# Kernel optimization log

Measured on AMD Instinct MI355X. Metric: run time of the kernel, lower is better.

## Reference

```python
import jax, jax.numpy as jnp
import numpy as np

N_NODES = 100000
N_EDGES = 1200000


def gcn_conv(h, W, b, src, dst, n_nodes):
    """PyG GCNConv: h' = D^-1/2 (A+I) D^-1/2 (h W) + b, with self-loops."""
    h = h @ W  # [N, out]
    # degree on A + I (count of incoming edges at dst, plus self-loop)
    deg = jnp.zeros((n_nodes,), h.dtype).at[dst].add(1.0) + 1.0
    dis = jax.lax.rsqrt(deg)  # deg^-1/2, deg >= 1 so safe
    norm = dis[src] * dis[dst]  # [E]
    out = jnp.zeros_like(h).at[dst].add(norm[:, None] * h[src])
    out = out + (1.0 / deg)[:, None] * h  # self-loop term: dis_i^2 * h_i
    return out + b


def global_features(x, T_norm):
    # matches compute_global_features; torch uses .item() so these are constants
    n_comp = jnp.sum(x[:, 2])
    n_AND = jnp.sum(x[:, 3])
    n_OR = jnp.sum(x[:, 4])
    mask = (x[:, 2] == 1.0).astype(x.dtype)
    msum = jnp.sum(mask)
    safe = jnp.maximum(msum, 1.0)
    avg_lambda = jnp.where(msum > 0, jnp.sum(x[:, 0] * mask) / safe, 0.0)
    avg_mu = jnp.where(msum > 0, jnp.sum(x[:, 1] * mask) / safe, 0.0)
    depth = n_AND + n_OR
    g = jnp.stack([n_comp, n_AND, n_OR, depth, avg_lambda, avg_mu, T_norm])[None, :]
    return jax.lax.stop_gradient(g)


def setup_inputs() -> dict:
    key = jax.random.key(0)
    ks = jax.random.split(key, 8)
    x = jax.random.normal(ks[0], (N_NODES, 5), jnp.float32)
    edge_index = jax.random.randint(ks[1], (2, N_EDGES), 0, N_NODES, jnp.int64)
    sc = lambda f: 1.0 / np.sqrt(f)
    return {
        "x": x,
        "edge_index": edge_index,
        "W1": jax.random.normal(ks[2], (5, 64), jnp.float32) * sc(5),
        "b1": jnp.zeros((64,), jnp.float32),
        "W2": jax.random.normal(ks[3], (64, 64), jnp.float32) * sc(64),
        "b2": jnp.zeros((64,), jnp.float32),
        "Wp1": jax.random.normal(ks[4], (71, 32), jnp.float32) * sc(71),
        "bp1": jnp.zeros((32,), jnp.float32),
        "Wp2": jax.random.normal(ks[5], (32, 2), jnp.float32) * sc(32),
        "bp2": jnp.zeros((2,), jnp.float32),
        "T": 100,
        "T_max": 500,
    }


def reference(x, edge_index, W1, b1, W2, b2, Wp1, bp1, Wp2, bp2, T, T_max):
    src, dst = edge_index[0], edge_index[1]
    n = x.shape[0]
    h = jax.nn.relu(gcn_conv(x, W1, b1, src, dst, n))
    h = jax.nn.relu(gcn_conv(h, W2, b2, src, dst, n))
    embedding = jnp.mean(h, axis=0, keepdims=True)  # global_mean_pool, single graph
    T_norm = jnp.asarray(T, x.dtype) / jnp.asarray(T_max, x.dtype)
    g = global_features(x, T_norm)
    e = jnp.concatenate([embedding, g], axis=1)  # [1, 71]
    raw = jax.nn.relu(e @ Wp1 + bp1) @ Wp2 + bp2  # [1, 2]
    return 2.0 + jax.nn.sigmoid(raw) * 4.0
```

## Files before the change

kernel.cpp:

```cpp
#include <hip/hip_runtime.h>
#include <hip/hip_bf16.h>

#define N_NODES_C 100000
#define N_EDGES_C 1200000
#define NB2 98
#define SUBCAP2 1792

typedef unsigned int uint32;
typedef __attribute__((ext_vector_type(8))) short bf16x8;
typedef __attribute__((ext_vector_type(4))) float f32x4;
typedef __attribute__((ext_vector_type(2))) float f32x2;

__device__ __forceinline__ float bf_lo(uint32 u) { return __uint_as_float(u << 16); }
__device__ __forceinline__ float bf_hi(uint32 u) { return __uint_as_float(u & 0xffff0000u); }
__device__ __forceinline__ uint32 bf16r(float f) {
    uint32 u = __float_as_uint(f);
    return (u + 0x7fffu + ((u >> 16) & 1u)) >> 16;
}
__device__ __forceinline__ uint32 pack2(float lo, float hi) {
    return bf16r(lo) | (bf16r(hi) << 16);
}

__global__ void bucket_kernel(const int4* __restrict__ src4, const int4* __restrict__ dst4,
                              int* __restrict__ bcnt, uint32* __restrict__ bedges, int nE4) {
    __shared__ int cntL[NB2];
    __shared__ int baseL[NB2];
    int tid = threadIdx.x;
    int i = blockIdx.x * 256 + tid;
    int sub = blockIdx.x & 7;
    for (int t = tid; t < NB2; t += 256) cntL[t] = 0;
    __syncthreads();
    int4 s4 = make_int4(0, 0, 0, 0), d4 = make_int4(0, 0, 0, 0);
    int b0 = 0, b1 = 0, b2 = 0, b3 = 0;
    bool act = i < nE4;
    if (act) {
        s4 = src4[i];
        d4 = dst4[i];
        b0 = d4.x >> 10; b1 = d4.y >> 10; b2 = d4.z >> 10; b3 = d4.w >> 10;
        atomicAdd(&cntL[b0], 1); atomicAdd(&cntL[b1], 1);
        atomicAdd(&cntL[b2], 1); atomicAdd(&cntL[b3], 1);
    }
    __syncthreads();
    for (int t = tid; t < NB2; t += 256) {
        int n = cntL[t];
        baseL[t] = n ? atomicAdd(&bcnt[sub * NB2 + t], n) : 0;
    }
    __syncthreads();
    for (int t = tid; t < NB2; t += 256) cntL[t] = 0;
    __syncthreads();
    if (act) {
        int o, slot;
        o = atomicAdd(&cntL[b0], 1); slot = baseL[b0] + o;
        if (slot < SUBCAP2)
            bedges[((size_t)b0 * 8 + sub) * SUBCAP2 + slot] =
                (uint32)s4.x | ((uint32)(d4.x & 1023) << 17);
        o = atomicAdd(&cntL[b1], 1); slot = baseL[b1] + o;
        if (slot < SUBCAP2)
            bedges[((size_t)b1 * 8 + sub) * SUBCAP2 + slot] =
                (uint32)s4.y | ((uint32)(d4.y & 1023) << 17);
        o = atomicAdd(&cntL[b2], 1); slot = baseL[b2] + o;
        if (slot < SUBCAP2)
            bedges[((size_t)b2 * 8 + sub) * SUBCAP2 + slot] =
                (uint32)s4.z | ((uint32)(d4.z & 1023) << 17);
        o = atomicAdd(&cntL[b3], 1); slot = baseL[b3] + o;
        if (slot < SUBCAP2)
            bedges[((size_t)b3 * 8 + sub) * SUBCAP2 + slot] =
                (uint32)s4.w | ((uint32)(d4.w & 1023) << 17);
    }
}

__global__ void bscan2_kernel(const int* __restrict__ bcnt, int* __restrict__ boff) {
    __shared__ int sm[128];
    int tid = threadIdx.x;
    int t = 0;
    if (tid < NB2) {
#pragma unroll
        for (int s = 0; s < 8; ++s) t += bcnt[s * NB2 + tid];
    }
    sm[tid] = t;
    __syncthreads();
    for (int off = 1; off < 128; off <<= 1) {
        int v = (tid >= off) ? sm[tid - off] : 0;
        __syncthreads();
        sm[tid] += v;
        __syncthreads();
    }
    if (tid < NB2) boff[tid] = sm[tid] - t;
}

__global__ void __launch_bounds__(1024)
bin3_kernel(const uint32* __restrict__ bedges, const int* __restrict__ bcnt,
            const int* __restrict__ boff, int* __restrict__ rowptr,
            float* __restrict__ dis, int* __restrict__ csr_src, int nN) {
    __shared__ int lc[1024];
    __shared__ int sm[1024];
    __shared__ int pr[1024];
    __shared__ int ln[8];
    int b = blockIdx.x;
    int tid = threadIdx.x;
    lc[tid] = 0;
    if (tid < 8) ln[tid] = min(bcnt[tid * NB2 + b], SUBCAP2);
    __syncthreads();
    const uint32* be = bedges + (size_t)b * 8 * SUBCAP2;
#pragma unroll
    for (int s = 0; s < 8; ++s) {
        int n = ln[s];
        const uint32* bs = be + s * SUBCAP2;
        for (int i = tid; i < n; i += 1024) atomicAdd(&lc[bs[i] >> 17], 1);
    }
    __syncthreads();
    int myc = lc[tid];
    sm[tid] = myc;
    __syncthreads();
    for (int off = 1; off < 1024; off <<= 1) {
        int v = (tid >= off) ? sm[tid - off] : 0;
        __syncthreads();
        sm[tid] += v;
        __syncthreads();
    }
    int excl = sm[tid] - myc;
    int base = boff[b];
    pr[tid] = base + excl;
    int node = (b << 10) + tid;
    if (node <= nN) rowptr[node] = base + excl;
    if (node < nN) dis[node] = rsqrtf((float)(myc + 1));
    lc[tid] = 0;
    __syncthreads();
#pragma unroll
    for (int s = 0; s < 8; ++s) {
        int n = ln[s];
        const uint32* bs = be + s * SUBCAP2;
        for (int i = tid; i < n; i += 1024) {
            uint32 ed = bs[i];
            int dlow = ed >> 17;
            int slot = pr[dlow] + atomicAdd(&lc[dlow], 1);
            csr_src[slot] = ed & 0x1FFFF;
        }
    }
}

__global__ void lin1_kernel(const float* __restrict__ x, const float* __restrict__ W1,
                            const float* __restrict__ dis, uint32* __restrict__ hlin, int nN) {
    __shared__ float Ws[320];
    int tid = threadIdx.x;
    if (tid < 256) Ws[tid] = W1[tid];
    if (tid < 64)  Ws[256 + tid] = W1[256 + tid];
    __syncthreads();
    int q = tid & 15;
    int sub = tid >> 4;
    for (int node = blockIdx.x * 16 + sub; node < nN; node += gridDim.x * 16) {
        const float* xr = x + node * 5;
        float x0 = xr[0], x1 = xr[1], x2 = xr[2], x3 = xr[3], x4 = xr[4];
        float dn = dis[node];
        int j = 4 * q;
        float a0 = x0 * Ws[j+0] + x1 * Ws[64+j+0] + x2 * Ws[128+j+0] + x3 * Ws[192+j+0] + x4 * Ws[256+j+0];
        float a1 = x0 * Ws[j+1] + x1 * Ws[64+j+1] + x2 * Ws[128+j+1] + x3 * Ws[192+j+1] + x4 * Ws[256+j+1];
        float a2 = x0 * Ws[j+2] + x1 * Ws[64+j+2] + x2 * Ws[128+j+2] + x3 * Ws[192+j+2] + x4 * Ws[256+j+2];
        float a3 = x0 * Ws[j+3] + x1 * Ws[64+j+3] + x2 * Ws[128+j+3] + x3 * Ws[192+j+3] + x4 * Ws[256+j+3];
        uint32 w = 0;
        w = __builtin_amdgcn_cvt_pk_fp8_f32(a0 * dn, a1 * dn, w, 0);
        w = __builtin_amdgcn_cvt_pk_fp8_f32(a2 * dn, a3 * dn, w, 1);
        hlin[node * 16 + q] = w;
    }
}

template <bool EPI>
__global__ void gather_kernel(const int* __restrict__ rowptr, const int* __restrict__ csr_src,
                              const uint2* __restrict__ hin, const float* __restrict__ bias,
                              void* __restrict__ hout, int nN) {
    int tid = threadIdx.x;
    int lane = tid & 63;
    int wv = tid >> 6;
    int g = lane >> 3;
    int l = lane & 7;
    float bb0 = 0, bb1 = 0, bb2 = 0, bb3 = 0, bb4 = 0, bb5 = 0, bb6 = 0, bb7 = 0;
    if (EPI) {
        const float* bp = bias + 8 * l;
        bb0 = bp[0]; bb1 = bp[1]; bb2 = bp[2]; bb3 = bp[3];
        bb4 = bp[4]; bb5 = bp[5]; bb6 = bp[6]; bb7 = bp[7];
    }
    int stride = gridDim.x * 32;
    for (int node = blockIdx.x * 32 + wv * 8 + g; node < nN; node += stride) {
        int e0 = rowptr[node];
        int e1 = rowptr[node + 1];
        float a0 = 0, a1 = 0, a2 = 0, a3 = 0, a4 = 0, a5 = 0, a6 = 0, a7 = 0;
        int e = e0;
        for (; e + 2 <= e1; e += 2) {
            int s0 = csr_src[e];
            int s1 = csr_src[e + 1];
            uint2 h0 = hin[(size_t)s0 * 8 + l];
            uint2 h1 = hin[(size_t)s1 * 8 + l];
            f32x2 p0 = __builtin_amdgcn_cvt_pk_f32_fp8(h0.x, 0);
            f32x2 p1 = __builtin_amdgcn_cvt_pk_f32_fp8(h0.x, 1);
            f32x2 p2 = __builtin_amdgcn_cvt_pk_f32_fp8(h0.y, 0);
            f32x2 p3 = __builtin_amdgcn_cvt_pk_f32_fp8(h0.y, 1);
            f32x2 q0 = __builtin_amdgcn_cvt_pk_f32_fp8(h1.x, 0);
            f32x2 q1 = __builtin_amdgcn_cvt_pk_f32_fp8(h1.x, 1);
            f32x2 q2 = __builtin_amdgcn_cvt_pk_f32_fp8(h1.y, 0);
            f32x2 q3 = __builtin_amdgcn_cvt_pk_f32_fp8(h1.y, 1);
            a0 += p0.x + q0.x; a1 += p0.y + q0.y;
            a2 += p1.x + q1.x; a3 += p1.y + q1.y;
            a4 += p2.x + q2.x; a5 += p2.y + q2.y;
            a6 += p3.x + q3.x; a7 += p3.y + q3.y;
        }
        if (e < e1) {
            int s0 = csr_src[e];
            uint2 h0 = hin[(size_t)s0 * 8 + l];
            f32x2 p0 = __builtin_amdgcn_cvt_pk_f32_fp8(h0.x, 0);
            f32x2 p1 = __builtin_amdgcn_cvt_pk_f32_fp8(h0.x, 1);
            f32x2 p2 = __builtin_amdgcn_cvt_pk_f32_fp8(h0.y, 0);
            f32x2 p3 = __builtin_amdgcn_cvt_pk_f32_fp8(h0.y, 1);
            a0 += p0.x; a1 += p0.y; a2 += p1.x; a3 += p1.y;
            a4 += p2.x; a5 += p2.y; a6 += p3.x; a7 += p3.y;
        }
        float dn = rsqrtf((float)(e1 - e0 + 1));
        uint2 hs = hin[(size_t)node * 8 + l];
        {
            f32x2 p0 = __builtin_amdgcn_cvt_pk_f32_fp8(hs.x, 0);
            f32x2 p1 = __builtin_amdgcn_cvt_pk_f32_fp8(hs.x, 1);
            f32x2 p2 = __builtin_amdgcn_cvt_pk_f32_fp8(hs.y, 0);
            f32x2 p3 = __builtin_amdgcn_cvt_pk_f32_fp8(hs.y, 1);
            a0 = (a0 + p0.x) * dn; a1 = (a1 + p0.y) * dn;
            a2 = (a2 + p1.x) * dn; a3 = (a3 + p1.y) * dn;
            a4 = (a4 + p2.x) * dn; a5 = (a5 + p2.y) * dn;
            a6 = (a6 + p3.x) * dn; a7 = (a7 + p3.y) * dn;
        }
        if (EPI) {
            a0 = fmaxf(a0 + bb0, 0.0f) * dn; a1 = fmaxf(a1 + bb1, 0.0f) * dn;
            a2 = fmaxf(a2 + bb2, 0.0f) * dn; a3 = fmaxf(a3 + bb3, 0.0f) * dn;
            a4 = fmaxf(a4 + bb4, 0.0f) * dn; a5 = fmaxf(a5 + bb5, 0.0f) * dn;
            a6 = fmaxf(a6 + bb6, 0.0f) * dn; a7 = fmaxf(a7 + bb7, 0.0f) * dn;
            uint32 w0 = 0, w1 = 0;
            w0 = __builtin_amdgcn_cvt_pk_fp8_f32(a0, a1, w0, 0);
            w0 = __builtin_amdgcn_cvt_pk_fp8_f32(a2, a3, w0, 1);
            w1 = __builtin_amdgcn_cvt_pk_fp8_f32(a4, a5, w1, 0);
            w1 = __builtin_amdgcn_cvt_pk_fp8_f32(a6, a7, w1, 1);
            ((uint2*)hout)[(size_t)node * 8 + l] = make_uint2(w0, w1);
        } else {
            ((uint4*)hout)[(size_t)node * 8 + l] = make_uint4(pack2(a0, a1), pack2(a2, a3),
                                                              pack2(a4, a5), pack2(a6, a7));
        }
    }
}

__global__ void lin2pool_kernel(const uint2* __restrict__ z2, const float* __restrict__ W2,
                                const float* __restrict__ b2, float* __restrict__ colsumB,
                                int nTiles) {
    int tid = threadIdx.x;
    int lane = tid & 63;
    int wv = tid >> 6;
    int l16 = lane & 15;
    int kg = lane >> 4;

    bf16x8 Bf[2][4];
#pragma unroll
    for (int ks = 0; ks < 2; ++ks)
#pragma unroll
        for (int t = 0; t < 4; ++t) {
            bf16x8 bb;
#pragma unroll
            for (int r = 0; r < 8; ++r) {
                int k = ks * 32 + kg * 8 + r;
                bb[r] = (short)bf16r(W2[k * 64 + t * 16 + l16]);
            }
            Bf[ks][t] = bb;
        }
    float bbias[4];
#pragma unroll
    for (int t = 0; t < 4; ++t) bbias[t] = b2[t * 16 + l16];

    float colacc[4][4];
#pragma unroll
    for (int t = 0; t < 4; ++t)
#pragma unroll
        for (int r = 0; r < 4; ++r) colacc[t][r] = 0.0f;

    for (int tile = blockIdx.x * 4 + wv; tile < nTiles; tile += gridDim.x * 4) {
        int nodeBase = tile * 16;
        const uint4* zrow = (const uint4*)(z2 + (size_t)(nodeBase + l16) * 16);
        uint4 A0u = zrow[kg];
        uint4 A1u = zrow[4 + kg];
        union { uint4 u; bf16x8 b; } c0, c1;
        c0.u = A0u; c1.u = A1u;
        f32x4 acc0 = {0, 0, 0, 0}, acc1 = {0, 0, 0, 0}, acc2 = {0, 0, 0, 0}, acc3 = {0, 0, 0, 0};
        acc0 = __builtin_amdgcn_mfma_f32_16x16x32_bf16(c0.b, Bf[0][0], acc0, 0, 0, 0);
        acc1 = __builtin_amdgcn_mfma_f32_16x16x32_bf16(c0.b, Bf[0][1], acc1, 0, 0, 0);
        acc2 = __builtin_amdgcn_mfma_f32_16x16x32_bf16(c0.b, Bf[0][2], acc2, 0, 0, 0);
        acc3 = __builtin_amdgcn_mfma_f32_16x16x32_bf16(c0.b, Bf[0][3], acc3, 0, 0, 0);
        acc0 = __builtin_amdgcn_mfma_f32_16x16x32_bf16(c1.b, Bf[1][0], acc0, 0, 0, 0);
        acc1 = __builtin_amdgcn_mfma_f32_16x16x32_bf16(c1.b, Bf[1][1], acc1, 0, 0, 0);
        acc2 = __builtin_amdgcn_mfma_f32_16x16x32_bf16(c1.b, Bf[1][2], acc2, 0, 0, 0);
        acc3 = __builtin_amdgcn_mfma_f32_16x16x32_bf16(c1.b, Bf[1][3], acc3, 0, 0, 0);
#pragma unroll
        for (int r = 0; r < 4; ++r) {
            colacc[0][r] += fmaxf(acc0[r] + bbias[0], 0.0f);
            colacc[1][r] += fmaxf(acc1[r] + bbias[1], 0.0f);
            colacc[2][r] += fmaxf(acc2[r] + bbias[2], 0.0f);
            colacc[3][r] += fmaxf(acc3[r] + bbias[3], 0.0f);
        }
    }
    float s[4];
#pragma unroll
    for (int t = 0; t < 4; ++t) {
        s[t] = colacc[t][0] + colacc[t][1] + colacc[t][2] + colacc[t][3];
        s[t] += __shfl_down(s[t], 32);
        s[t] += __shfl_down(s[t], 16);
    }
    __shared__ float sm[4][64];
    if (lane < 16) {
#pragma unroll
        for (int t = 0; t < 4; ++t) sm[wv][t * 16 + lane] = s[t];
    }
    __syncthreads();
    if (tid < 64) {
        float v = sm[0][tid] + sm[1][tid] + sm[2][tid] + sm[3][tid];
        atomicAdd(&colsumB[(blockIdx.x & 15) * 64 + tid], v);
    }
}

__global__ void gfeat_kernel(const float* __restrict__ x, float* __restrict__ gsB, int nN) {
    int tid = threadIdx.x;
    int i = blockIdx.x * 256 + tid;
    float s0 = 0, s1 = 0, s2 = 0, s3 = 0, s4 = 0, s5 = 0;
    if (i < nN) {
        const float* xr = x + i * 5;
        float x0 = xr[0], x1 = xr[1], x2 = xr[2], x3 = xr[3], x4 = xr[4];
        float m = (x2 == 1.0f) ? 1.0f : 0.0f;
        s0 = x0 * m; s1 = x1 * m; s2 = x2; s3 = x3; s4 = x4; s5 = m;
    }
#pragma unroll
    for (int off = 32; off > 0; off >>= 1) {
        s0 += __shfl_down(s0, off);
        s1 += __shfl_down(s1, off);
        s2 += __shfl_down(s2, off);
        s3 += __shfl_down(s3, off);
        s4 += __shfl_down(s4, off);
        s5 += __shfl_down(s5, off);
    }
    __shared__ float smg[4][6];
    if ((tid & 63) == 0) {
        int w = tid >> 6;
        smg[w][0] = s0; smg[w][1] = s1; smg[w][2] = s2;
        smg[w][3] = s3; smg[w][4] = s4; smg[w][5] = s5;
    }
    __syncthreads();
    if (tid < 6) {
        float s = smg[0][tid] + smg[1][tid] + smg[2][tid] + smg[3][tid];
        atomicAdd(&gsB[(blockIdx.x & 15) * 16 + tid], s);
    }
}

__global__ void head_kernel(const float* __restrict__ colsumB, const float* __restrict__ gsB,
                            const float* __restrict__ Wp1, const float* __restrict__ bp1,
                            const float* __restrict__ Wp2, const float* __restrict__ bp2,
                            const int* __restrict__ T, const int* __restrict__ Tmax,
                            float* __restrict__ out) {
    __shared__ float e[71];
    __shared__ float gsum[6];
    __shared__ float hid[32];
    int tid = threadIdx.x;
    if (tid < 64) {
        float s = 0.0f;
#pragma unroll
        for (int r = 0; r < 16; ++r) s += colsumB[r * 64 + tid];
        e[tid] = s * (1.0f / (float)N_NODES_C);
    } else if (tid < 70) {
        int k = tid - 64;
        float s = 0.0f;
#pragma unroll
        for (int r = 0; r < 16; ++r) s += gsB[r * 16 + k];
        gsum[k] = s;
    }
    __syncthreads();
    if (tid == 0) {
        e[64] = gsum[2];
        e[65] = gsum[3];
        e[66] = gsum[4];
        e[67] = gsum[3] + gsum[4];
        float m = gsum[5];
        e[68] = (m > 0.0f) ? gsum[0] / fmaxf(m, 1.0f) : 0.0f;
        e[69] = (m > 0.0f) ? gsum[1] / fmaxf(m, 1.0f) : 0.0f;
        e[70] = (float)T[0] / (float)Tmax[0];
    }
    __syncthreads();
    if (tid < 32) {
        float acc = bp1[tid];
        for (int i = 0; i < 71; ++i) acc += e[i] * Wp1[i * 32 + tid];
        hid[tid] = fmaxf(acc, 0.0f);
    }
    __syncthreads();
    if (tid < 2) {
        float acc = bp2[tid];
        for (int k = 0; k < 32; ++k) acc += hid[k] * Wp2[k * 2 + tid];
        out[tid] = 2.0f + 4.0f / (1.0f + expf(-acc));
    }
}

extern "C" void kernel_launch(void* const* d_in, const int* in_sizes, int n_in,
                              void* d_out, int out_size, void* d_ws, size_t ws_size,
                              hipStream_t stream) {
    const float* x    = (const float*)d_in[0];
    const int*   ei   = (const int*)d_in[1];
    const float* W1   = (const float*)d_in[2];
    const float* b1   = (const float*)d_in[3];
    const float* W2   = (const float*)d_in[4];
    const float* b2   = (const float*)d_in[5];
    const float* Wp1  = (const float*)d_in[6];
    const float* bp1  = (const float*)d_in[7];
    const float* Wp2  = (const float*)d_in[8];
    const float* bp2  = (const float*)d_in[9];
    const int*   T    = (const int*)d_in[10];
    const int*   Tmax = (const int*)d_in[11];
    float* out = (float*)d_out;

    const int nN = N_NODES_C;
    const int nE = N_EDGES_C;
    const int* src = ei;
    const int* dst = ei + nE;

    char* ws = (char*)d_ws;
    int*    bcnt    = (int*)   (ws + 0);
    float*  colsumB = (float*) (ws + 3136);
    float*  gsB     = (float*) (ws + 7232);
    int*    boff    = (int*)   (ws + 8256);
    int*    rowptr  = (int*)   (ws + 8768);
    float*  dis     = (float*) (ws + 408784);
    int*    csr_src = (int*)   (ws + 808784);
    uint32* bedges  = (uint32*)(ws + 5608784);
    uint32* hlin1   = (uint32*)(ws + 11228496);
    uint32* h1      = (uint32*)(ws + 17628496);
    uint32* z2      = (uint32*)(ws + 24028496);

    hipMemsetAsync(ws, 0, 8256, stream);

    bucket_kernel<<<(nE / 4 + 255) / 256, 256, 0, stream>>>(
        (const int4*)src, (const int4*)dst, bcnt, bedges, nE / 4);
    bscan2_kernel<<<1, 128, 0, stream>>>(bcnt, boff);
    bin3_kernel<<<NB2, 1024, 0, stream>>>(bedges, bcnt, boff, rowptr, dis, csr_src, nN);

    lin1_kernel<<<1024, 256, 0, stream>>>(x, W1, dis, hlin1, nN);
    gather_kernel<true><<<2048, 256, 0, stream>>>(rowptr, csr_src, (const uint2*)hlin1, b1,
                                                  (void*)h1, nN);

    gather_kernel<false><<<2048, 256, 0, stream>>>(rowptr, csr_src, (const uint2*)h1, nullptr,
                                                   (void*)z2, nN);
    lin2pool_kernel<<<512, 256, 0, stream>>>((const uint2*)z2, W2, b2, colsumB, nN / 16);

    gfeat_kernel<<<(nN + 255) / 256, 256, 0, stream>>>(x, gsB, nN);

    head_kernel<<<1, 128, 0, stream>>>(colsumB, gsB, Wp1, bp1, Wp2, bp2, T, Tmax, out);
}
```

Baseline: 184.0 us.

## Fuse bucket scan and first linear layer into CSR bin kernel; store z2 as fp8

Folds the separate bucket-offset scan kernel and the lin1 kernel into the CSR binning kernel. Each of the 98 blocks now recomputes the bucket prefix scan and computes the 5x64 projection for its own nodes, scaled by the degree it just counted, so the dis array and two launches go away. The second gather now writes z2 as fp8 instead of bf16, which halves its write and the lin2pool read, and lin2pool converts fp8 to bf16 before the MFMA. In exchange, lin1 now runs on only 98 blocks with one thread per node doing 64 outputs, which lowers parallelism, and the extra fp8 rounding loses precision.

```diff
diff --git a/kernel.cpp b/kernel.cpp
--- a/kernel.cpp
+++ b/kernel.cpp
@@ -11,14 +11,22 @@
 typedef __attribute__((ext_vector_type(4))) float f32x4;
 typedef __attribute__((ext_vector_type(2))) float f32x2;
 
-__device__ __forceinline__ float bf_lo(uint32 u) { return __uint_as_float(u << 16); }
-__device__ __forceinline__ float bf_hi(uint32 u) { return __uint_as_float(u & 0xffff0000u); }
 __device__ __forceinline__ uint32 bf16r(float f) {
     uint32 u = __float_as_uint(f);
     return (u + 0x7fffu + ((u >> 16) & 1u)) >> 16;
 }
 __device__ __forceinline__ uint32 pack2(float lo, float hi) {
     return bf16r(lo) | (bf16r(hi) << 16);
+}
+__device__ __forceinline__ bf16x8 fp8x8_to_bf16x8(uint2 u) {
+    f32x2 p0 = __builtin_amdgcn_cvt_pk_f32_fp8(u.x, 0);
+    f32x2 p1 = __builtin_amdgcn_cvt_pk_f32_fp8(u.x, 1);
+    f32x2 p2 = __builtin_amdgcn_cvt_pk_f32_fp8(u.y, 0);
+    f32x2 p3 = __builtin_amdgcn_cvt_pk_f32_fp8(u.y, 1);
+    union { uint32 w[4]; bf16x8 b; } r;
+    r.w[0] = pack2(p0.x, p0.y); r.w[1] = pack2(p1.x, p1.y);
+    r.w[2] = pack2(p2.x, p2.y); r.w[3] = pack2(p3.x, p3.y);
+    return r.b;
 }
 
 __global__ void bucket_kernel(const int4* __restrict__ src4, const int4* __restrict__ dst4,
@@ -69,44 +77,44 @@
     }
 }
 
-__global__ void bscan2_kernel(const int* __restrict__ bcnt, int* __restrict__ boff) {
-    __shared__ int sm[128];
-    int tid = threadIdx.x;
-    int t = 0;
-    if (tid < NB2) {
-#pragma unroll
-        for (int s = 0; s < 8; ++s) t += bcnt[s * NB2 + tid];
-    }
-    sm[tid] = t;
-    __syncthreads();
-    for (int off = 1; off < 128; off <<= 1) {
-        int v = (tid >= off) ? sm[tid - off] : 0;
-        __syncthreads();
-        sm[tid] += v;
-        __syncthreads();
-    }
-    if (tid < NB2) boff[tid] = sm[tid] - t;
-}
-
 __global__ void __launch_bounds__(1024)
-bin3_kernel(const uint32* __restrict__ bedges, const int* __restrict__ bcnt,
-            const int* __restrict__ boff, int* __restrict__ rowptr,
-            float* __restrict__ dis, int* __restrict__ csr_src, int nN) {
+bin4_kernel(const uint32* __restrict__ bedges, const int* __restrict__ bcnt,
+            const float* __restrict__ x, const float* __restrict__ W1,
+            int* __restrict__ rowptr, uint32* __restrict__ hlin,
+            int* __restrict__ csr_src, int nN) {
     __shared__ int lc[1024];
     __shared__ int sm[1024];
     __shared__ int pr[1024];
+    __shared__ int bs[128];
     __shared__ int ln[8];
+    __shared__ int baseSh;
+    __shared__ float Ws[320];
     int b = blockIdx.x;
     int tid = threadIdx.x;
     lc[tid] = 0;
+    if (tid < 320) Ws[tid] = W1[tid];
     if (tid < 8) ln[tid] = min(bcnt[tid * NB2 + b], SUBCAP2);
-    __syncthreads();
+    if (tid < 128) {
+        int t = 0;
+        if (tid < NB2)
+#pragma unroll
+            for (int s = 0; s < 8; ++s) t += bcnt[s * NB2 + tid];
+        bs[tid] = t;
+    }
+    __syncthreads();
+    for (int off = 1; off < 128; off <<= 1) {
+        int v = (tid < 128 && tid >= off) ? bs[tid - off] : 0;
+        __syncthreads();
+        if (tid < 128) bs[tid] += v;
+        __syncthreads();
+    }
+    if (tid == 0) baseSh = b ? bs[b - 1] : 0;
     const uint32* be = bedges + (size_t)b * 8 * SUBCAP2;
 #pragma unroll
     for (int s = 0; s < 8; ++s) {
         int n = ln[s];
-        const uint32* bs = be + s * SUBCAP2;
-        for (int i = tid; i < n; i += 1024) atomicAdd(&lc[bs[i] >> 17], 1);
+        const uint32* bsrc = be + s * SUBCAP2;
+        for (int i = tid; i < n; i += 1024) atomicAdd(&lc[bsrc[i] >> 17], 1);
     }
     __syncthreads();
     int myc = lc[tid];
@@ -118,20 +126,42 @@
         sm[tid] += v;
         __syncthreads();
     }
+    int base = baseSh;
     int excl = sm[tid] - myc;
-    int base = boff[b];
     pr[tid] = base + excl;
     int node = (b << 10) + tid;
     if (node <= nN) rowptr[node] = base + excl;
-    if (node < nN) dis[node] = rsqrtf((float)(myc + 1));
+    if (node < nN) {
+        const float* xr = x + (size_t)node * 5;
+        float x0 = xr[0], x1 = xr[1], x2 = xr[2], x3 = xr[3], x4 = xr[4];
+        float dn = rsqrtf((float)(myc + 1));
+        uint32 w[16];
+#pragma unroll
+        for (int q = 0; q < 16; ++q) {
+            int j = q * 4;
+            float a0 = x0 * Ws[j+0] + x1 * Ws[64+j+0] + x2 * Ws[128+j+0] + x3 * Ws[192+j+0] + x4 * Ws[256+j+0];
+            float a1 = x0 * Ws[j+1] + x1 * Ws[64+j+1] + x2 * Ws[128+j+1] + x3 * Ws[192+j+1] + x4 * Ws[256+j+1];
+            float a2 = x0 * Ws[j+2] + x1 * Ws[64+j+2] + x2 * Ws[128+j+2] + x3 * Ws[192+j+2] + x4 * Ws[256+j+2];
+            float a3 = x0 * Ws[j+3] + x1 * Ws[64+j+3] + x2 * Ws[128+j+3] + x3 * Ws[192+j+3] + x4 * Ws[256+j+3];
+            uint32 ww = 0;
+            ww = __builtin_amdgcn_cvt_pk_fp8_f32(a0 * dn, a1 * dn, ww, 0);
+            ww = __builtin_amdgcn_cvt_pk_fp8_f32(a2 * dn, a3 * dn, ww, 1);
+            w[q] = ww;
+        }
+        uint4* dstp = (uint4*)(hlin + (size_t)node * 16);
+        dstp[0] = make_uint4(w[0], w[1], w[2], w[3]);
+        dstp[1] = make_uint4(w[4], w[5], w[6], w[7]);
+        dstp[2] = make_uint4(w[8], w[9], w[10], w[11]);
+        dstp[3] = make_uint4(w[12], w[13], w[14], w[15]);
+    }
     lc[tid] = 0;
     __syncthreads();
 #pragma unroll
     for (int s = 0; s < 8; ++s) {
         int n = ln[s];
-        const uint32* bs = be + s * SUBCAP2;
+        const uint32* bsrc = be + s * SUBCAP2;
         for (int i = tid; i < n; i += 1024) {
-            uint32 ed = bs[i];
+            uint32 ed = bsrc[i];
             int dlow = ed >> 17;
             int slot = pr[dlow] + atomicAdd(&lc[dlow], 1);
             csr_src[slot] = ed & 0x1FFFF;
@@ -139,35 +169,10 @@
     }
 }
 
-__global__ void lin1_kernel(const float* __restrict__ x, const float* __restrict__ W1,
-                            const float* __restrict__ dis, uint32* __restrict__ hlin, int nN) {
-    __shared__ float Ws[320];
-    int tid = threadIdx.x;
-    if (tid < 256) Ws[tid] = W1[tid];
-    if (tid < 64)  Ws[256 + tid] = W1[256 + tid];
-    __syncthreads();
-    int q = tid & 15;
-    int sub = tid >> 4;
-    for (int node = blockIdx.x * 16 + sub; node < nN; node += gridDim.x * 16) {
-        const float* xr = x + node * 5;
-        float x0 = xr[0], x1 = xr[1], x2 = xr[2], x3 = xr[3], x4 = xr[4];
-        float dn = dis[node];
-        int j = 4 * q;
-        float a0 = x0 * Ws[j+0] + x1 * Ws[64+j+0] + x2 * Ws[128+j+0] + x3 * Ws[192+j+0] + x4 * Ws[256+j+0];
-        float a1 = x0 * Ws[j+1] + x1 * Ws[64+j+1] + x2 * Ws[128+j+1] + x3 * Ws[192+j+1] + x4 * Ws[256+j+1];
-        float a2 = x0 * Ws[j+2] + x1 * Ws[64+j+2] + x2 * Ws[128+j+2] + x3 * Ws[192+j+2] + x4 * Ws[256+j+2];
-        float a3 = x0 * Ws[j+3] + x1 * Ws[64+j+3] + x2 * Ws[128+j+3] + x3 * Ws[192+j+3] + x4 * Ws[256+j+3];
-        uint32 w = 0;
-        w = __builtin_amdgcn_cvt_pk_fp8_f32(a0 * dn, a1 * dn, w, 0);
-        w = __builtin_amdgcn_cvt_pk_fp8_f32(a2 * dn, a3 * dn, w, 1);
-        hlin[node * 16 + q] = w;
-    }
-}
-
 template <bool EPI>
 __global__ void gather_kernel(const int* __restrict__ rowptr, const int* __restrict__ csr_src,
                               const uint2* __restrict__ hin, const float* __restrict__ bias,
-                              void* __restrict__ hout, int nN) {
+                              uint2* __restrict__ hout, int nN) {
     int tid = threadIdx.x;
     int lane = tid & 63;
     int wv = tid >> 6;
@@ -230,16 +235,13 @@
             a2 = fmaxf(a2 + bb2, 0.0f) * dn; a3 = fmaxf(a3 + bb3, 0.0f) * dn;
             a4 = fmaxf(a4 + bb4, 0.0f) * dn; a5 = fmaxf(a5 + bb5, 0.0f) * dn;
             a6 = fmaxf(a6 + bb6, 0.0f) * dn; a7 = fmaxf(a7 + bb7, 0.0f) * dn;
-            uint32 w0 = 0, w1 = 0;
-            w0 = __builtin_amdgcn_cvt_pk_fp8_f32(a0, a1, w0, 0);
-            w0 = __builtin_amdgcn_cvt_pk_fp8_f32(a2, a3, w0, 1);
-            w1 = __builtin_amdgcn_cvt_pk_fp8_f32(a4, a5, w1, 0);
-            w1 = __builtin_amdgcn_cvt_pk_fp8_f32(a6, a7, w1, 1);
-            ((uint2*)hout)[(size_t)node * 8 + l] = make_uint2(w0, w1);
-        } else {
-            ((uint4*)hout)[(size_t)node * 8 + l] = make_uint4(pack2(a0, a1), pack2(a2, a3),
-                                                              pack2(a4, a5), pack2(a6, a7));
-        }
+        }
+        uint32 w0 = 0, w1 = 0;
+        w0 = __builtin_amdgcn_cvt_pk_fp8_f32(a0, a1, w0, 0);
+        w0 = __builtin_amdgcn_cvt_pk_fp8_f32(a2, a3, w0, 1);
+        w1 = __builtin_amdgcn_cvt_pk_fp8_f32(a4, a5, w1, 0);
+        w1 = __builtin_amdgcn_cvt_pk_fp8_f32(a6, a7, w1, 1);
+        hout[(size_t)node * 8 + l] = make_uint2(w0, w1);
     }
 }
 
@@ -277,20 +279,18 @@
 
     for (int tile = blockIdx.x * 4 + wv; tile < nTiles; tile += gridDim.x * 4) {
         int nodeBase = tile * 16;
-        const uint4* zrow = (const uint4*)(z2 + (size_t)(nodeBase + l16) * 16);
-        uint4 A0u = zrow[kg];
-        uint4 A1u = zrow[4 + kg];
-        union { uint4 u; bf16x8 b; } c0, c1;
-        c0.u = A0u; c1.u = A1u;
+        const uint2* zrow = z2 + (size_t)(nodeBase + l16) * 8;
+        bf16x8 A0 = fp8x8_to_bf16x8(zrow[kg]);
+        bf16x8 A1 = fp8x8_to_bf16x8(zrow[4 + kg]);
         f32x4 acc0 = {0, 0, 0, 0}, acc1 = {0, 0, 0, 0}, acc2 = {0, 0, 0, 0}, acc3 = {0, 0, 0, 0};
-        acc0 = __builtin_amdgcn_mfma_f32_16x16x32_bf16(c0.b, Bf[0][0], acc0, 0, 0, 0);
-        acc1 = __builtin_amdgcn_mfma_f32_16x16x32_bf16(c0.b, Bf[0][1], acc1, 0, 0, 0);
-        acc2 = __builtin_amdgcn_mfma_f32_16x16x32_bf16(c0.b, Bf[0][2], acc2, 0, 0, 0);
-        acc3 = __builtin_amdgcn_mfma_f32_16x16x32_bf16(c0.b, Bf[0][3], acc3, 0, 0, 0);
-        acc0 = __builtin_amdgcn_mfma_f32_16x16x32_bf16(c1.b, Bf[1][0], acc0, 0, 0, 0);
-        acc1 = __builtin_amdgcn_mfma_f32_16x16x32_bf16(c1.b, Bf[1][1], acc1, 0, 0, 0);
-        acc2 = __builtin_amdgcn_mfma_f32_16x16x32_bf16(c1.b, Bf[1][2], acc2, 0, 0, 0);
-        acc3 = __builtin_amdgcn_mfma_f32_16x16x32_bf16(c1.b, Bf[1][3], acc3, 0, 0, 0);
+        acc0 = __builtin_amdgcn_mfma_f32_16x16x32_bf16(A0, Bf[0][0], acc0, 0, 0, 0);
+        acc1 = __builtin_amdgcn_mfma_f32_16x16x32_bf16(A0, Bf[0][1], acc1, 0, 0, 0);
+        acc2 = __builtin_amdgcn_mfma_f32_16x16x32_bf16(A0, Bf[0][2], acc2, 0, 0, 0);
+        acc3 = __builtin_amdgcn_mfma_f32_16x16x32_bf16(A0, Bf[0][3], acc3, 0, 0, 0);
+        acc0 = __builtin_amdgcn_mfma_f32_16x16x32_bf16(A1, Bf[1][0], acc0, 0, 0, 0);
+        acc1 = __builtin_amdgcn_mfma_f32_16x16x32_bf16(A1, Bf[1][1], acc1, 0, 0, 0);
+        acc2 = __builtin_amdgcn_mfma_f32_16x16x32_bf16(A1, Bf[1][2], acc2, 0, 0, 0);
+        acc3 = __builtin_amdgcn_mfma_f32_16x16x32_bf16(A1, Bf[1][3], acc3, 0, 0, 0);
 #pragma unroll
         for (int r = 0; r < 4; ++r) {
             colacc[0][r] += fmaxf(acc0[r] + bbias[0], 0.0f);
@@ -422,28 +422,24 @@
     int*    bcnt    = (int*)   (ws + 0);
     float*  colsumB = (float*) (ws + 3136);
     float*  gsB     = (float*) (ws + 7232);
-    int*    boff    = (int*)   (ws + 8256);
-    int*    rowptr  = (int*)   (ws + 8768);
-    float*  dis     = (float*) (ws + 408784);
-    int*    csr_src = (int*)   (ws + 808784);
-    uint32* bedges  = (uint32*)(ws + 5608784);
-    uint32* hlin1   = (uint32*)(ws + 11228496);
-    uint32* h1      = (uint32*)(ws + 17628496);
-    uint32* z2      = (uint32*)(ws + 24028496);
+    int*    rowptr  = (int*)   (ws + 8256);
+    int*    csr_src = (int*)   (ws + 408272);
+    uint32* bedges  = (uint32*)(ws + 5208272);
+    uint32* hlin1   = (uint32*)(ws + 10827984);
+    uint32* h1      = (uint32*)(ws + 17227984);
+    uint32* z2      = (uint32*)(ws + 23627984);
 
     hipMemsetAsync(ws, 0, 8256, stream);
 
     bucket_kernel<<<(nE / 4 + 255) / 256, 256, 0, stream>>>(
         (const int4*)src, (const int4*)dst, bcnt, bedges, nE / 4);
-    bscan2_kernel<<<1, 128, 0, stream>>>(bcnt, boff);
-    bin3_kernel<<<NB2, 1024, 0, stream>>>(bedges, bcnt, boff, rowptr, dis, csr_src, nN);
-
-    lin1_kernel<<<1024, 256, 0, stream>>>(x, W1, dis, hlin1, nN);
+    bin4_kernel<<<NB2, 1024, 0, stream>>>(bedges, bcnt, x, W1, rowptr, hlin1, csr_src, nN);
+
     gather_kernel<true><<<2048, 256, 0, stream>>>(rowptr, csr_src, (const uint2*)hlin1, b1,
-                                                  (void*)h1, nN);
+                                                  (uint2*)h1, nN);
 
     gather_kernel<false><<<2048, 256, 0, stream>>>(rowptr, csr_src, (const uint2*)h1, nullptr,
-                                                   (void*)z2, nN);
+                                                   (uint2*)z2, nN);
     lin2pool_kernel<<<512, 256, 0, stream>>>((const uint2*)z2, W2, b2, colsumB, nN / 16);
 
     gfeat_kernel<<<(nN + 255) / 256, 256, 0, stream>>>(x, gsB, nN);
```

Measured after the change: 180.0 us. -2.2%, faster.
